# Kernel tuning notes

Measured on AMD Instinct MI355X. Metric: run time of the kernel, lower is better.

Reference implementation:

```python
import jax, jax.numpy as jnp
import numpy as np

N_NODES = 50000
N_EDGES = 800000
D_IN = 256
DIM_H = 256
N_GRAPHS = 500
N_OUT = 10
BN_EPS = 1e-5


def _mlp(h, W1, b1, gamma, beta, mean, var, W2, b2):
    # Linear -> BatchNorm1d (eval, running stats) -> ReLU -> Linear -> ReLU
    h = h @ W1 + b1
    h = (h - mean) * (gamma / jnp.sqrt(var + BN_EPS)) + beta
    h = jax.nn.relu(h)
    return jax.nn.relu(h @ W2 + b2)


def _gin_conv(x, src, dst, params):
    # PyG GINConv with eps=0: out = nn(x + sum_{j in N(i)} x_j)
    agg = jax.ops.segment_sum(x[src], dst, num_segments=N_NODES)
    return _mlp(x + agg, *params)


def setup_inputs() -> dict:
    key = jax.random.key(0)
    ks = jax.random.split(key, 24)
    x = jax.random.normal(ks[0], (N_NODES, D_IN), dtype=jnp.float32)
    edge_index = jax.random.randint(ks[1], (2, N_EDGES), 0, N_NODES, dtype=jnp.int64)
    batch = jnp.sort(jax.random.randint(ks[2], (N_NODES,), 0, N_GRAPHS, dtype=jnp.int64))

    def lin(k, fan_in, fan_out):
        s = 1.0 / np.sqrt(fan_in)
        kw, kb = jax.random.split(k)
        W = jax.random.uniform(kw, (fan_in, fan_out), minval=-s, maxval=s, dtype=jnp.float32)
        b = jax.random.uniform(kb, (fan_out,), minval=-s, maxval=s, dtype=jnp.float32)
        return W, b

    def bn(k, d):
        k1, k2, k3, k4 = jax.random.split(k, 4)
        gamma = 1.0 + 0.1 * jax.random.normal(k1, (d,), dtype=jnp.float32)
        beta = 0.1 * jax.random.normal(k2, (d,), dtype=jnp.float32)
        mean = 0.1 * jax.random.normal(k3, (d,), dtype=jnp.float32)
        var = jax.random.uniform(k4, (d,), minval=0.5, maxval=1.5, dtype=jnp.float32)
        return gamma, beta, mean, var

    W1a, b1a = lin(ks[3], D_IN, DIM_H)
    g1a, be1a, m1a, v1a = bn(ks[4], DIM_H)
    W2a, b2a = lin(ks[5], DIM_H, DIM_H)
    W1b, b1b = lin(ks[6], DIM_H, DIM_H)
    g1b, be1b, m1b, v1b = bn(ks[7], DIM_H)
    W2b, b2b = lin(ks[8], DIM_H, DIM_H)
    lin1_W, lin1_b = lin(ks[9], DIM_H * 2, DIM_H * 3)
    lin2_W, lin2_b = lin(ks[10], DIM_H * 3, N_OUT)

    return dict(x=x, edge_index=edge_index, batch=batch,
                W1a=W1a, b1a=b1a, g1a=g1a, be1a=be1a, m1a=m1a, v1a=v1a, W2a=W2a, b2a=b2a,
                W1b=W1b, b1b=b1b, g1b=g1b, be1b=be1b, m1b=m1b, v1b=v1b, W2b=W2b, b2b=b2b,
                lin1_W=lin1_W, lin1_b=lin1_b, lin2_W=lin2_W, lin2_b=lin2_b)


def reference(x, edge_index, batch,
              W1a, b1a, g1a, be1a, m1a, v1a, W2a, b2a,
              W1b, b1b, g1b, be1b, m1b, v1b, W2b, b2b,
              lin1_W, lin1_b, lin2_W, lin2_b):
    src, dst = edge_index[0], edge_index[1]
    h1 = _gin_conv(x, src, dst, (W1a, b1a, g1a, be1a, m1a, v1a, W2a, b2a))
    h2 = _gin_conv(h1, src, dst, (W1b, b1b, g1b, be1b, m1b, v1b, W2b, b2b))
    p1 = jax.ops.segment_sum(h1, batch, num_segments=N_GRAPHS)  # global_add_pool
    p2 = jax.ops.segment_sum(h2, batch, num_segments=N_GRAPHS)
    h = jnp.concatenate([p1, p2], axis=1)
    h = jax.nn.relu(h @ lin1_W + lin1_b)
    # dropout p=0.6 is identity in eval mode
    h = h @ lin2_W + lin2_b
    return jax.nn.log_softmax(h, axis=1)
```

## Files before the change

kernel.cpp:

```cpp
#include <hip/hip_runtime.h>

#define N_NODES 50000
#define MPAD 50176
#define N_EDGES 800000
#define DIM 256
#define N_GRAPHS 500
#define N_OUT 10
#define BN_EPS 1e-5f
#define SCAN_BS 1024
#define KSPLIT 4

typedef unsigned int u32;
typedef short bf16x8 __attribute__((ext_vector_type(8)));
typedef unsigned short us8 __attribute__((ext_vector_type(8)));
typedef float f32x4 __attribute__((ext_vector_type(4)));

typedef __attribute__((address_space(1))) const unsigned int gas_u32;
typedef __attribute__((address_space(3))) unsigned int las_u32;

__device__ inline void g2l16(const void* g, void* l) {
    __builtin_amdgcn_global_load_lds((gas_u32*)g, (las_u32*)l, 16, 0, 0);
}

__device__ inline float b2f(unsigned short u) {
    union { u32 i; float f; } c; c.i = ((u32)u) << 16; return c.f;
}
__device__ inline unsigned short f2b(float f) {
    u32 x = __builtin_bit_cast(u32, f);
    return (unsigned short)((x + 0x7FFFu + ((x >> 16) & 1u)) >> 16);
}

__global__ void zero_i(int* __restrict__ p, int n) {
    int i = blockIdx.x * blockDim.x + threadIdx.x;
    if (i < n) p[i] = 0;
}
__global__ void hist_dst(const int* __restrict__ dst, int* __restrict__ deg) {
    int e = blockIdx.x * blockDim.x + threadIdx.x;
    if (e < N_EDGES) atomicAdd(&deg[dst[e]], 1);
}
__global__ void scan_phase1(const int* __restrict__ deg, int* __restrict__ rowptr,
                            int* __restrict__ bsum, int n) {
    __shared__ int sh[SCAN_BS];
    int i = blockIdx.x * SCAN_BS + threadIdx.x;
    int v = (i < n) ? deg[i] : 0;
    sh[threadIdx.x] = v;
    __syncthreads();
    for (int off = 1; off < SCAN_BS; off <<= 1) {
        int t = (threadIdx.x >= off) ? sh[threadIdx.x - off] : 0;
        __syncthreads();
        sh[threadIdx.x] += t;
        __syncthreads();
    }
    if (i < n) rowptr[i] = sh[threadIdx.x] - v;
    if (threadIdx.x == SCAN_BS - 1) bsum[blockIdx.x] = sh[threadIdx.x];
}
__global__ void scan_phase2(int* __restrict__ bsum, int nb) {
    if (threadIdx.x == 0 && blockIdx.x == 0) {
        int run = 0;
        for (int b = 0; b < nb; b++) { int v = bsum[b]; bsum[b] = run; run += v; }
    }
}
__global__ void scan_phase3(int* __restrict__ rowptr, int* __restrict__ cursor,
                            const int* __restrict__ bsum, int n) {
    int i = blockIdx.x * SCAN_BS + threadIdx.x;
    if (i < n) {
        int v = rowptr[i] + bsum[blockIdx.x];
        rowptr[i] = v;
        cursor[i] = v;
    }
    if (i == 0) rowptr[n] = N_EDGES;
}
__global__ void fill_csr(const int* __restrict__ src, const int* __restrict__ dst,
                         int* __restrict__ cursor, int* __restrict__ col) {
    int e = blockIdx.x * blockDim.x + threadIdx.x;
    if (e < N_EDGES) {
        int p = atomicAdd(&cursor[dst[e]], 1);
        col[p] = src[e];
    }
}
__global__ void graph_starts(const int* __restrict__ batch, int* __restrict__ gstart) {
    int g = blockIdx.x * blockDim.x + threadIdx.x;
    if (g > N_GRAPHS) return;
    if (g == N_GRAPHS) { gstart[g] = N_NODES; return; }
    int lo = 0, hi = N_NODES;
    while (lo < hi) { int mid = (lo + hi) >> 1; if (batch[mid] < g) lo = mid + 1; else hi = mid; }
    gstart[g] = lo;
}

__global__ void conv_x(const float4* __restrict__ in, ushort4* __restrict__ out, int n4) {
    int i = blockIdx.x * blockDim.x + threadIdx.x;
    if (i < n4) {
        float4 v = in[i];
        ushort4 o; o.x = f2b(v.x); o.y = f2b(v.y); o.z = f2b(v.z); o.w = f2b(v.w);
        out[i] = o;
    }
}
__global__ void conv_wt4(const float* __restrict__ W0, const float* __restrict__ W1,
                         const float* __restrict__ W2, const float* __restrict__ W3,
                         unsigned short* __restrict__ Wt) {
    int mat = blockIdx.y;
    const float* W = (mat == 0) ? W0 : (mat == 1) ? W1 : (mat == 2) ? W2 : W3;
    int n = blockIdx.x;
    int k = threadIdx.x;
    Wt[((size_t)mat << 16) + (size_t)n * 256 + k] = f2b(W[(size_t)k * 256 + n]);
}
__global__ void make_ss(const float* __restrict__ bias, const float* __restrict__ gamma,
                        const float* __restrict__ beta, const float* __restrict__ mean,
                        const float* __restrict__ var, float* __restrict__ scale,
                        float* __restrict__ shift, int has_bn) {
    int i = threadIdx.x;
    if (has_bn) {
        float s = gamma[i] * rsqrtf(var[i] + BN_EPS);
        scale[i] = s;
        shift[i] = (bias[i] - mean[i]) * s + beta[i];
    } else {
        scale[i] = 1.f;
        shift[i] = bias[i];
    }
}

__global__ void gather_bf(const unsigned short* __restrict__ feat,
                          const int* __restrict__ col,
                          const int* __restrict__ rowptr,
                          unsigned short* __restrict__ out) {
    int node = blockIdx.x * 4 + (threadIdx.x >> 6);
    if (node >= N_NODES) return;
    int lane = threadIdx.x & 63;
    int half = lane >> 5;
    int d8 = (lane & 31) * 8;
    float acc[8];
    #pragma unroll
    for (int j = 0; j < 8; j++) acc[j] = 0.f;
    if (half == 0) {
        us8 own = *reinterpret_cast<const us8*>(&feat[(size_t)node * DIM + d8]);
        #pragma unroll
        for (int j = 0; j < 8; j++) acc[j] = b2f((unsigned short)own[j]);
    }
    int s = rowptr[node], e = rowptr[node + 1];
    int i = s + half;
    for (; i + 6 < e; i += 8) {
        int n0 = col[i], n1 = col[i + 2], n2 = col[i + 4], n3 = col[i + 6];
        us8 v0 = *reinterpret_cast<const us8*>(&feat[(size_t)n0 * DIM + d8]);
        us8 v1 = *reinterpret_cast<const us8*>(&feat[(size_t)n1 * DIM + d8]);
        us8 v2 = *reinterpret_cast<const us8*>(&feat[(size_t)n2 * DIM + d8]);
        us8 v3 = *reinterpret_cast<const us8*>(&feat[(size_t)n3 * DIM + d8]);
        #pragma unroll
        for (int j = 0; j < 8; j++)
            acc[j] += (b2f((unsigned short)v0[j]) + b2f((unsigned short)v1[j]))
                    + (b2f((unsigned short)v2[j]) + b2f((unsigned short)v3[j]));
    }
    for (; i < e; i += 2) {
        int n0 = col[i];
        us8 v0 = *reinterpret_cast<const us8*>(&feat[(size_t)n0 * DIM + d8]);
        #pragma unroll
        for (int j = 0; j < 8; j++) acc[j] += b2f((unsigned short)v0[j]);
    }
    #pragma unroll
    for (int j = 0; j < 8; j++) acc[j] += __shfl_xor(acc[j], 32, 64);
    if (half == 0) {
        us8 o;
        #pragma unroll
        for (int j = 0; j < 8; j++) o[j] = (short)f2b(acc[j]);
        *reinterpret_cast<us8*>(&out[(size_t)node * DIM + d8]) = o;
    }
}

__global__ __launch_bounds__(512)
void gemm_bf16(const unsigned short* __restrict__ A,
               const unsigned short* __restrict__ Wt,
               const float* __restrict__ scale,
               const float* __restrict__ shift,
               unsigned short* __restrict__ C, int M) {
    __shared__ unsigned short Asb[128 * 32];
    __shared__ unsigned short Bsb[256 * 32];
    int t = threadIdx.x;
    int wave = t >> 6, lane = t & 63;
    int m0 = blockIdx.x * 128;
    int wr = (wave >> 2) * 64;
    int wc = (wave & 3) * 64;

    f32x4 acc[4][4];
    #pragma unroll
    for (int m = 0; m < 4; m++)
        #pragma unroll
        for (int n = 0; n < 4; n++)
            acc[m][n] = (f32x4){0.f, 0.f, 0.f, 0.f};

    int rsel = lane & 15;
    int ksel = (lane >> 4) * 8;

    for (int k0 = 0; k0 < 256; k0 += 32) {
        {
            int row = t >> 2, cb = (t & 3) * 16;
            g2l16((const char*)A + (size_t)(m0 + row) * 512 + (size_t)k0 * 2 + cb,
                  (char*)Asb + (size_t)t * 16);
        }
        #pragma unroll
        for (int i = 0; i < 2; i++) {
            int slot = i * 512 + t;
            int row = slot >> 2, cb = (slot & 3) * 16;
            g2l16((const char*)Wt + (size_t)row * 512 + (size_t)k0 * 2 + cb,
                  (char*)Bsb + (size_t)slot * 16);
        }
        __syncthreads();

        bf16x8 af[4], bfr[4];
        #pragma unroll
        for (int m = 0; m < 4; m++)
            af[m] = *(const bf16x8*)&Asb[(size_t)(wr + m * 16 + rsel) * 32 + ksel];
        #pragma unroll
        for (int n = 0; n < 4; n++)
            bfr[n] = *(const bf16x8*)&Bsb[(size_t)(wc + n * 16 + rsel) * 32 + ksel];
        #pragma unroll
        for (int m = 0; m < 4; m++)
            #pragma unroll
            for (int n = 0; n < 4; n++)
                acc[m][n] = __builtin_amdgcn_mfma_f32_16x16x32_bf16(af[m], bfr[n], acc[m][n], 0, 0, 0);
        __syncthreads();
    }

    int cr = lane >> 4;
    #pragma unroll
    for (int n = 0; n < 4; n++) {
        int colg = wc + n * 16 + rsel;
        float s = scale[colg], sh = shift[colg];
        #pragma unroll
        for (int m = 0; m < 4; m++) {
            int rowb = m0 + wr + m * 16 + cr * 4;
            #pragma unroll
            for (int r = 0; r < 4; r++) {
                int row = rowb + r;
                if (row < M) {
                    float v = fmaxf(acc[m][n][r] * s + sh, 0.f);
                    C[(size_t)row * 256 + colg] = f2b(v);
                }
            }
        }
    }
}

__global__ void pool_seg(const unsigned short* __restrict__ h1,
                         const unsigned short* __restrict__ h2,
                         const int* __restrict__ gstart,
                         float* __restrict__ pcat) {
    int g = blockIdx.x;
    int t = threadIdx.x;
    int s = gstart[g], e = gstart[g + 1];
    float a1 = 0.f, a2 = 0.f;
    for (int n = s; n < e; n++) {
        a1 += b2f(h1[(size_t)n * DIM + t]);
        a2 += b2f(h2[(size_t)n * DIM + t]);
    }
    pcat[(size_t)g * 512 + t]       = a1;
    pcat[(size_t)g * 512 + 256 + t] = a2;
}

__global__ void head1(const float* __restrict__ A,
                      const float* __restrict__ W1,
                      float* __restrict__ Hpart) {
    __shared__ float As[16][65];
    __shared__ float Bs[16][65];
    int t = threadIdx.x;
    int m0 = blockIdx.y * 64;
    int n0 = blockIdx.x * 64;
    int kz = blockIdx.z * (512 / KSPLIT);
    int tx = t & 15, ty = t >> 4;
    float acc[4][4] = {};
    for (int k0 = kz; k0 < kz + 512 / KSPLIT; k0 += 16) {
        #pragma unroll
        for (int i = 0; i < 4; i++) {
            int r = (t >> 4) + i * 16;
            int k = t & 15;
            int gr = m0 + r;
            As[k][r] = (gr < N_GRAPHS) ? A[(size_t)gr * 512 + k0 + k] : 0.f;
        }
        #pragma unroll
        for (int i = 0; i < 4; i++) {
            int k = (t >> 6) + i * 4;
            int n = t & 63;
            Bs[k][n] = W1[(size_t)(k0 + k) * 768 + n0 + n];
        }
        __syncthreads();
        #pragma unroll
        for (int k = 0; k < 16; k++) {
            float a[4], b[4];
            #pragma unroll
            for (int i = 0; i < 4; i++) a[i] = As[k][ty * 4 + i];
            #pragma unroll
            for (int j = 0; j < 4; j++) b[j] = Bs[k][tx * 4 + j];
            #pragma unroll
            for (int i = 0; i < 4; i++)
                #pragma unroll
                for (int j = 0; j < 4; j++)
                    acc[i][j] += a[i] * b[j];
        }
        __syncthreads();
    }
    float* Hz = Hpart + (size_t)blockIdx.z * N_GRAPHS * 768;
    #pragma unroll
    for (int i = 0; i < 4; i++) {
        int gm = m0 + ty * 4 + i;
        if (gm >= N_GRAPHS) continue;
        #pragma unroll
        for (int j = 0; j < 4; j++) {
            int gn = n0 + tx * 4 + j;
            Hz[(size_t)gm * 768 + gn] = acc[i][j];
        }
    }
}

__global__ void head2(const float* __restrict__ Hpart, const float* __restrict__ b1,
                      const float* __restrict__ W2, const float* __restrict__ b2,
                      float* __restrict__ out) {
    int g = blockIdx.x;
    int lane = threadIdx.x;
    float part[N_OUT];
    #pragma unroll
    for (int o = 0; o < N_OUT; o++) part[o] = 0.f;
    for (int k = lane; k < 768; k += 64) {
        float hv = b1[k];
        #pragma unroll
        for (int z = 0; z < KSPLIT; z++)
            hv += Hpart[((size_t)z * N_GRAPHS + g) * 768 + k];
        hv = fmaxf(hv, 0.f);
        #pragma unroll
        for (int o = 0; o < N_OUT; o++) part[o] += hv * W2[(size_t)k * N_OUT + o];
    }
    #pragma unroll
    for (int o = 0; o < N_OUT; o++) {
        #pragma unroll
        for (int off = 32; off > 0; off >>= 1)
            part[o] += __shfl_down(part[o], off, 64);
    }
    if (lane == 0) {
        float logits[N_OUT];
        float mx = -1e30f;
        #pragma unroll
        for (int o = 0; o < N_OUT; o++) { logits[o] = part[o] + b2[o]; mx = fmaxf(mx, logits[o]); }
        float ssum = 0.f;
        #pragma unroll
        for (int o = 0; o < N_OUT; o++) ssum += expf(logits[o] - mx);
        float lse = logf(ssum);
        #pragma unroll
        for (int o = 0; o < N_OUT; o++)
            out[(size_t)g * N_OUT + o] = logits[o] - mx - lse;
    }
}

extern "C" void kernel_launch(void* const* d_in, const int* in_sizes, int n_in,
                              void* d_out, int out_size, void* d_ws, size_t ws_size,
                              hipStream_t stream) {
    const float* x     = (const float*)d_in[0];
    const int*   ei    = (const int*)d_in[1];
    const int*   batch = (const int*)d_in[2];
    const float* W1a = (const float*)d_in[3];
    const float* b1a = (const float*)d_in[4];
    const float* g1a = (const float*)d_in[5];
    const float* be1a= (const float*)d_in[6];
    const float* m1a = (const float*)d_in[7];
    const float* v1a = (const float*)d_in[8];
    const float* W2a = (const float*)d_in[9];
    const float* b2a = (const float*)d_in[10];
    const float* W1b = (const float*)d_in[11];
    const float* b1b = (const float*)d_in[12];
    const float* g1b = (const float*)d_in[13];
    const float* be1b= (const float*)d_in[14];
    const float* m1b = (const float*)d_in[15];
    const float* v1b = (const float*)d_in[16];
    const float* W2b = (const float*)d_in[17];
    const float* b2b = (const float*)d_in[18];
    const float* lin1_W = (const float*)d_in[19];
    const float* lin1_b = (const float*)d_in[20];
    const float* lin2_W = (const float*)d_in[21];
    const float* lin2_b = (const float*)d_in[22];

    const size_t NBUF = (size_t)MPAD * DIM;
    char* ws = (char*)d_ws;
    unsigned short* agg  = (unsigned short*)ws;            ws += NBUF * 2;
    unsigned short* mid  = (unsigned short*)ws;            ws += NBUF * 2;
    unsigned short* h1   = (unsigned short*)ws;            ws += NBUF * 2;
    unsigned short* h2   = (unsigned short*)ws;            ws += NBUF * 2;
    unsigned short* x_bf = (unsigned short*)ws;            ws += (size_t)N_NODES * DIM * 2;
    unsigned short* Wt   = (unsigned short*)ws;            ws += 4 * 65536 * 2;
    float* ss    = (float*)ws;                             ws += 8 * 256 * 4;
    float* pcat  = (float*)ws;                             ws += (size_t)N_GRAPHS * 512 * 4;
    float* Hpart = (float*)ws;                             ws += (size_t)KSPLIT * N_GRAPHS * 768 * 4;
    int* deg     = (int*)ws;                               ws += (size_t)N_NODES * 4;
    int* cursor  = (int*)ws;                               ws += (size_t)N_NODES * 4;
    int* rowptr  = (int*)ws;                               ws += (size_t)(N_NODES + 1) * 4;
    int* bsum    = (int*)ws;                               ws += 64 * 4;
    int* col     = (int*)ws;                               ws += (size_t)N_EDGES * 4;
    int* gstart  = (int*)ws;

    const int* srcE = ei;
    const int* dstE = ei + N_EDGES;

    const int nscan = (N_NODES + SCAN_BS - 1) / SCAN_BS;

    zero_i<<<(N_NODES + 255) / 256, 256, 0, stream>>>(deg, N_NODES);
    hist_dst<<<(N_EDGES + 255) / 256, 256, 0, stream>>>(dstE, deg);
    scan_phase1<<<nscan, SCAN_BS, 0, stream>>>(deg, rowptr, bsum, N_NODES);
    scan_phase2<<<1, 64, 0, stream>>>(bsum, nscan);
    scan_phase3<<<nscan, SCAN_BS, 0, stream>>>(rowptr, cursor, bsum, N_NODES);
    fill_csr<<<(N_EDGES + 255) / 256, 256, 0, stream>>>(srcE, dstE, cursor, col);
    graph_starts<<<2, 256, 0, stream>>>(batch, gstart);

    conv_x<<<(N_NODES * DIM / 4 + 255) / 256, 256, 0, stream>>>(
        (const float4*)x, (ushort4*)x_bf, N_NODES * DIM / 4);
    dim3 wt_grid(256, 4);
    conv_wt4<<<wt_grid, 256, 0, stream>>>(W1a, W2a, W1b, W2b, Wt);
    make_ss<<<1, 256, 0, stream>>>(b1a, g1a, be1a, m1a, v1a, ss + 0 * 512, ss + 0 * 512 + 256, 1);
    make_ss<<<1, 256, 0, stream>>>(b2a, nullptr, nullptr, nullptr, nullptr, ss + 1 * 512, ss + 1 * 512 + 256, 0);
    make_ss<<<1, 256, 0, stream>>>(b1b, g1b, be1b, m1b, v1b, ss + 2 * 512, ss + 2 * 512 + 256, 1);
    make_ss<<<1, 256, 0, stream>>>(b2b, nullptr, nullptr, nullptr, nullptr, ss + 3 * 512, ss + 3 * 512 + 256, 0);

    gather_bf<<<(N_NODES + 3) / 4, 256, 0, stream>>>(x_bf, col, rowptr, agg);
    gemm_bf16<<<MPAD / 128, 512, 0, stream>>>(agg, Wt + 0 * 65536, ss + 0 * 512, ss + 0 * 512 + 256, mid, N_NODES);
    gemm_bf16<<<MPAD / 128, 512, 0, stream>>>(mid, Wt + 1 * 65536, ss + 1 * 512, ss + 1 * 512 + 256, h1, N_NODES);

    gather_bf<<<(N_NODES + 3) / 4, 256, 0, stream>>>(h1, col, rowptr, agg);
    gemm_bf16<<<MPAD / 128, 512, 0, stream>>>(agg, Wt + 2 * 65536, ss + 2 * 512, ss + 2 * 512 + 256, mid, N_NODES);
    gemm_bf16<<<MPAD / 128, 512, 0, stream>>>(mid, Wt + 3 * 65536, ss + 3 * 512, ss + 3 * 512 + 256, h2, N_NODES);

    pool_seg<<<N_GRAPHS, 256, 0, stream>>>(h1, h2, gstart, pcat);
    dim3 h1grid(12, 8, KSPLIT);
    head1<<<h1grid, 256, 0, stream>>>(pcat, lin1_W, Hpart);
    head2<<<N_GRAPHS, 64, 0, stream>>>(Hpart, lin1_b, lin2_W, lin2_b, (float*)d_out);
}
```

Before: 395.9 us.

## Double-buffer GEMM LDS tiles and deepen gather unroll in aggregation

The bf16 GEMM now keeps two LDS buffers for the A and B tiles and issues the global-to-LDS loads for the next K-step before computing on the current one. This drops one barrier per iteration and lets load latency overlap the MFMA work. The aggregation kernel's neighbour gather loop is unrolled from 4 to 8 loads in flight per half-wave to expose more memory parallelism. The costs are double the LDS for the GEMM, which may reduce occupancy, and higher register pressure in the gather kernel.

New measurement: 412.9 us. 4.3% more time.

```diff
diff --git a/kernel.cpp b/kernel.cpp
--- a/kernel.cpp
+++ b/kernel.cpp
@@ -138,16 +138,19 @@
     }
     int s = rowptr[node], e = rowptr[node + 1];
     int i = s + half;
-    for (; i + 6 < e; i += 8) {
-        int n0 = col[i], n1 = col[i + 2], n2 = col[i + 4], n3 = col[i + 6];
-        us8 v0 = *reinterpret_cast<const us8*>(&feat[(size_t)n0 * DIM + d8]);
-        us8 v1 = *reinterpret_cast<const us8*>(&feat[(size_t)n1 * DIM + d8]);
-        us8 v2 = *reinterpret_cast<const us8*>(&feat[(size_t)n2 * DIM + d8]);
-        us8 v3 = *reinterpret_cast<const us8*>(&feat[(size_t)n3 * DIM + d8]);
-        #pragma unroll
-        for (int j = 0; j < 8; j++)
-            acc[j] += (b2f((unsigned short)v0[j]) + b2f((unsigned short)v1[j]))
-                    + (b2f((unsigned short)v2[j]) + b2f((unsigned short)v3[j]));
+    for (; i + 14 < e; i += 16) {
+        int nn[8];
+        #pragma unroll
+        for (int q = 0; q < 8; q++) nn[q] = col[i + 2 * q];
+        us8 v[8];
+        #pragma unroll
+        for (int q = 0; q < 8; q++)
+            v[q] = *reinterpret_cast<const us8*>(&feat[(size_t)nn[q] * DIM + d8]);
+        #pragma unroll
+        for (int q = 0; q < 8; q++)
+            #pragma unroll
+            for (int j = 0; j < 8; j++)
+                acc[j] += b2f((unsigned short)v[q][j]);
     }
     for (; i < e; i += 2) {
         int n0 = col[i];
@@ -171,14 +174,19 @@
                const float* __restrict__ scale,
                const float* __restrict__ shift,
                unsigned short* __restrict__ C, int M) {
-    __shared__ unsigned short Asb[128 * 32];
-    __shared__ unsigned short Bsb[256 * 32];
+    __shared__ unsigned short Asb[2][128 * 32];
+    __shared__ unsigned short Bsb[2][256 * 32];
     int t = threadIdx.x;
     int wave = t >> 6, lane = t & 63;
     int m0 = blockIdx.x * 128;
     int wr = (wave >> 2) * 64;
     int wc = (wave & 3) * 64;
 
+    int cb = (t & 3) * 16;
+    const char* Ab  = (const char*)A  + (size_t)(m0 + (t >> 2)) * 512 + cb;
+    const char* Bb0 = (const char*)Wt + (size_t)(t >> 2) * 512 + cb;
+    const char* Bb1 = (const char*)Wt + (size_t)(128 + (t >> 2)) * 512 + cb;
+
     f32x4 acc[4][4];
     #pragma unroll
     for (int m = 0; m < 4; m++)
@@ -189,34 +197,35 @@
     int rsel = lane & 15;
     int ksel = (lane >> 4) * 8;
 
-    for (int k0 = 0; k0 < 256; k0 += 32) {
-        {
-            int row = t >> 2, cb = (t & 3) * 16;
-            g2l16((const char*)A + (size_t)(m0 + row) * 512 + (size_t)k0 * 2 + cb,
-                  (char*)Asb + (size_t)t * 16);
-        }
-        #pragma unroll
-        for (int i = 0; i < 2; i++) {
-            int slot = i * 512 + t;
-            int row = slot >> 2, cb = (slot & 3) * 16;
-            g2l16((const char*)Wt + (size_t)row * 512 + (size_t)k0 * 2 + cb,
-                  (char*)Bsb + (size_t)slot * 16);
-        }
-        __syncthreads();
-
+    g2l16(Ab,  (char*)Asb[0] + (size_t)t * 16);
+    g2l16(Bb0, (char*)Bsb[0] + (size_t)t * 16);
+    g2l16(Bb1, (char*)Bsb[0] + (size_t)(512 + t) * 16);
+    __syncthreads();
+
+    int cur = 0;
+    for (int ks = 0; ks < 8; ks++) {
+        if (ks < 7) {
+            size_t ko = (size_t)(ks + 1) * 64;
+            g2l16(Ab + ko,  (char*)Asb[cur ^ 1] + (size_t)t * 16);
+            g2l16(Bb0 + ko, (char*)Bsb[cur ^ 1] + (size_t)t * 16);
+            g2l16(Bb1 + ko, (char*)Bsb[cur ^ 1] + (size_t)(512 + t) * 16);
+        }
+        const unsigned short* As = Asb[cur];
+        const unsigned short* Bs = Bsb[cur];
         bf16x8 af[4], bfr[4];
         #pragma unroll
         for (int m = 0; m < 4; m++)
-            af[m] = *(const bf16x8*)&Asb[(size_t)(wr + m * 16 + rsel) * 32 + ksel];
+            af[m] = *(const bf16x8*)&As[(size_t)(wr + m * 16 + rsel) * 32 + ksel];
         #pragma unroll
         for (int n = 0; n < 4; n++)
-            bfr[n] = *(const bf16x8*)&Bsb[(size_t)(wc + n * 16 + rsel) * 32 + ksel];
+            bfr[n] = *(const bf16x8*)&Bs[(size_t)(wc + n * 16 + rsel) * 32 + ksel];
         #pragma unroll
         for (int m = 0; m < 4; m++)
             #pragma unroll
             for (int n = 0; n < 4; n++)
                 acc[m][n] = __builtin_amdgcn_mfma_f32_16x16x32_bf16(af[m], bfr[n], acc[m][n], 0, 0, 0);
         __syncthreads();
+        cur ^= 1;
     }
 
     int cr = lane >> 4;
```

## Double-buffer LDS tiles in bf16 GEMM with async prefetch two stages ahead

Applied to the files above, without the earlier changes.

Splits the GEMM's A and B shared-memory tiles into two buffers. While MFMAs run on the current K-slice, the global-to-LDS loads for a later slice are issued into the other buffer, using vmcnt waits and raw barriers in place of the two full __syncthreads per iteration. The goal is to hide global load latency behind compute. It doubles LDS use, which may lower occupancy, and it relies on hand-placed waitcnt values being correct.

Measured after the change: 395.3 us. No clear change (-0.2%).

```diff
diff --git a/kernel.cpp b/kernel.cpp
--- a/kernel.cpp
+++ b/kernel.cpp
@@ -171,14 +171,19 @@
                const float* __restrict__ scale,
                const float* __restrict__ shift,
                unsigned short* __restrict__ C, int M) {
-    __shared__ unsigned short Asb[128 * 32];
-    __shared__ unsigned short Bsb[256 * 32];
+    __shared__ unsigned short Asb[2][128 * 32];
+    __shared__ unsigned short Bsb[2][256 * 32];
     int t = threadIdx.x;
     int wave = t >> 6, lane = t & 63;
     int m0 = blockIdx.x * 128;
     int wr = (wave >> 2) * 64;
     int wc = (wave & 3) * 64;
 
+    int cb = (t & 3) * 16;
+    const char* Ab  = (const char*)A  + (size_t)(m0 + (t >> 2)) * 512 + cb;
+    const char* Bb0 = (const char*)Wt + (size_t)(t >> 2) * 512 + cb;
+    const char* Bb1 = (const char*)Wt + (size_t)(128 + (t >> 2)) * 512 + cb;
+
     f32x4 acc[4][4];
     #pragma unroll
     for (int m = 0; m < 4; m++)
@@ -189,34 +194,45 @@
     int rsel = lane & 15;
     int ksel = (lane >> 4) * 8;
 
-    for (int k0 = 0; k0 < 256; k0 += 32) {
-        {
-            int row = t >> 2, cb = (t & 3) * 16;
-            g2l16((const char*)A + (size_t)(m0 + row) * 512 + (size_t)k0 * 2 + cb,
-                  (char*)Asb + (size_t)t * 16);
-        }
-        #pragma unroll
-        for (int i = 0; i < 2; i++) {
-            int slot = i * 512 + t;
-            int row = slot >> 2, cb = (slot & 3) * 16;
-            g2l16((const char*)Wt + (size_t)row * 512 + (size_t)k0 * 2 + cb,
-                  (char*)Bsb + (size_t)slot * 16);
-        }
-        __syncthreads();
-
+    #pragma unroll
+    for (int p = 0; p < 2; p++) {
+        size_t ko = (size_t)p * 64;
+        g2l16(Ab + ko,  (char*)Asb[p] + (size_t)t * 16);
+        g2l16(Bb0 + ko, (char*)Bsb[p] + (size_t)t * 16);
+        g2l16(Bb1 + ko, (char*)Bsb[p] + (size_t)(512 + t) * 16);
+    }
+
+    #pragma unroll
+    for (int ks = 0; ks < 8; ks++) {
+        const int cur = ks & 1;
+        if (ks < 7) asm volatile("s_waitcnt vmcnt(3)" ::: "memory");
+        else        asm volatile("s_waitcnt vmcnt(0)" ::: "memory");
+        __builtin_amdgcn_s_barrier();
+        asm volatile("" ::: "memory");
+
+        const unsigned short* As = Asb[cur];
+        const unsigned short* Bs = Bsb[cur];
         bf16x8 af[4], bfr[4];
         #pragma unroll
         for (int m = 0; m < 4; m++)
-            af[m] = *(const bf16x8*)&Asb[(size_t)(wr + m * 16 + rsel) * 32 + ksel];
+            af[m] = *(const bf16x8*)&As[(size_t)(wr + m * 16 + rsel) * 32 + ksel];
         #pragma unroll
         for (int n = 0; n < 4; n++)
-            bfr[n] = *(const bf16x8*)&Bsb[(size_t)(wc + n * 16 + rsel) * 32 + ksel];
+            bfr[n] = *(const bf16x8*)&Bs[(size_t)(wc + n * 16 + rsel) * 32 + ksel];
         #pragma unroll
         for (int m = 0; m < 4; m++)
             #pragma unroll
             for (int n = 0; n < 4; n++)
                 acc[m][n] = __builtin_amdgcn_mfma_f32_16x16x32_bf16(af[m], bfr[n], acc[m][n], 0, 0, 0);
-        __syncthreads();
+
+        asm volatile("" ::: "memory");
+        __builtin_amdgcn_s_barrier();
+        if (ks + 2 < 8) {
+            size_t ko = (size_t)(ks + 2) * 64;
+            g2l16(Ab + ko,  (char*)Asb[cur] + (size_t)t * 16);
+            g2l16(Bb0 + ko, (char*)Bsb[cur] + (size_t)t * 16);
+            g2l16(Bb1 + ko, (char*)Bsb[cur] + (size_t)(512 + t) * 16);
+        }
     }
 
     int cr = lane >> 4;
```
